# Kernel optimization log

Hardware: AMD Instinct MI355X
Metric: run time of the kernel (lower is better)

Reference implementation:

```python
import jax, jax.numpy as jnp
import numpy as np

N = 50000          # number of nodes / output rows (len(degs))
IN_C, OUT_C = 16, 16
EDGE_F = 13        # edge feature dim fed to filter net
HID = 32           # filter-net hidden width
E_NOMINAL = 800000 # target number of edges (sum of degs)


def setup_inputs() -> dict:
    rng = np.random.default_rng(0)
    # variable per-node degrees in [0, 32], adjusted so they sum exactly to E_NOMINAL
    degs = rng.integers(0, 33, size=N).astype(np.int64)
    degs[0] = max(0, degs[0] + (E_NOMINAL - int(degs.sum())))
    E = int(degs.sum())
    # segment id of each edge = destination node (equivalent to the degs-driven loop)
    idxd = np.repeat(np.arange(N, dtype=np.int32), degs)
    idxn = rng.integers(0, N, size=E).astype(np.int32)  # source node gather index

    key = jax.random.key(0)
    k1, k2, k3, k4 = jax.random.split(key, 4)
    x = jax.random.normal(k1, (N, IN_C), jnp.float32)
    edgefeats = jax.random.normal(k2, (E, EDGE_F), jnp.float32)
    # filter net: Linear(EDGE_F->HID) -> ReLU -> Linear(HID->IN_C*OUT_C)
    W1 = jax.random.normal(k3, (EDGE_F, HID), jnp.float32) / np.float32(np.sqrt(EDGE_F))
    b1 = jnp.zeros((HID,), jnp.float32)
    W2 = jax.random.normal(k4, (HID, IN_C * OUT_C), jnp.float32) / np.float32(np.sqrt(HID))
    b2 = jnp.zeros((IN_C * OUT_C,), jnp.float32)
    return {
        "x": x, "edgefeats": edgefeats,
        "W1": W1, "b1": b1, "W2": W2, "b2": b2,
        "idxn": jnp.asarray(idxn), "idxd": jnp.asarray(idxd),
        "degs": jnp.asarray(degs.astype(np.float32)),
    }


def reference(x, edgefeats, W1, b1, W2, b2, idxn, idxd, degs):
    # filter net generates a per-edge [IN_C, OUT_C] weight matrix
    h = jax.nn.relu(edgefeats @ W1 + b1)                 # [E, HID]
    w = (h @ W2 + b2).reshape(-1, IN_C, OUT_C)           # [E, IN_C, OUT_C]
    # gather source-node features and apply per-edge matvec (bmm with [E,1,IN_C])
    sel = x[idxn]                                        # [E, IN_C]
    prod = jnp.einsum('ei,eio->eo', sel, w)              # [E, OUT_C]
    # segment-mean over each node's incoming edges; degree-0 nodes -> 0
    s = jax.ops.segment_sum(prod, idxd, num_segments=N)  # [N, OUT_C]
    d = degs[:, None]
    return jnp.where(d > 0, s / jnp.maximum(d, 1.0), jnp.float32(0.0))
```

## Files before the change

### kernel.cpp

```cpp
#include <hip/hip_runtime.h>

typedef _Float16 half2v __attribute__((ext_vector_type(2)));
typedef _Float16 half8v __attribute__((ext_vector_type(8)));
typedef float   float4v __attribute__((ext_vector_type(4)));

#define INC     16
#define OUTC    16
#define EFN     13
#define HIDC    32
#define EPB     512
#define NTILES  (EPB / 16)
#define MAXSPAN 128

union H8 { half8v v; half2v h2[4]; };

#define SB(t, l, j) (((t) * 64 + (l)) * 8 + (j))

__global__ __launch_bounds__(256) void edge_kernel(
    const float* __restrict__ x,
    const float* __restrict__ edgefeats,
    const float* __restrict__ W1,
    const float* __restrict__ b1,
    const float* __restrict__ W2,
    const float* __restrict__ b2,
    const int*   __restrict__ idxn,
    const int*   __restrict__ idxd,
    const float* __restrict__ degs,
    float*       __restrict__ out,
    float*       __restrict__ wsPfirst,
    float*       __restrict__ wsPlast,
    int*         __restrict__ wsMeta,
    int E)
{
    __shared__ __align__(16) _Float16 sB[16 * 64 * 8];
    __shared__ __align__(16) _Float16 sW1h[EFN * HIDC];
    __shared__ float         lacc[MAXSPAN * OUTC];
    __shared__ int           sidxn[EPB];
    __shared__ unsigned char su[EPB];

    const int tid  = threadIdx.x;
    const int lane = tid & 63;
    const int wid  = tid >> 6;
    const int n    = lane & 15;
    const int q    = lane >> 4;

    const long b0   = (long)blockIdx.x * EPB;
    const long bEnd = (b0 + EPB < (long)E) ? (b0 + EPB) : (long)E;
    const int  d_lo = idxd[b0];
    const int  d_hi = idxd[bEnd - 1];
    const int  span = d_hi - d_lo;

    #pragma unroll
    for (int it = 0; it < 8; ++it) {
        const int idx4 = tid + it * 256;
        const float4 w4 = ((const float4*)W2)[idx4];
        const int c0 = (idx4 * 4) & 255;
        const int kk = (idx4 * 4) >> 8;
        const int t  = c0 >> 4;
        const int l0 = ((kk >> 3) << 4) + (c0 & 15);
        const int j  = kk & 7;
        sB[SB(t, l0 + 0, j)] = (_Float16)w4.x;
        sB[SB(t, l0 + 1, j)] = (_Float16)w4.y;
        sB[SB(t, l0 + 2, j)] = (_Float16)w4.z;
        sB[SB(t, l0 + 3, j)] = (_Float16)w4.w;
    }
    for (int i = tid; i < EFN * HIDC; i += 256) sW1h[i] = (_Float16)W1[i];
    #pragma unroll
    for (int it = 0; it < MAXSPAN * OUTC / 256; ++it) lacc[tid + it * 256] = 0.0f;
    {
        const int i2 = tid * 2;
        long e0 = b0 + i2, e1 = b0 + i2 + 1;
        if (e0 >= (long)E) e0 = E - 1;
        if (e1 >= (long)E) e1 = E - 1;
        sidxn[i2]     = idxn[e0];
        sidxn[i2 + 1] = idxn[e1];
        const unsigned u0 = (unsigned)(idxd[e0] - d_lo);
        const unsigned u1 = (unsigned)(idxd[e1] - d_lo);
        *(unsigned short*)&su[i2] = (unsigned short)(u0 | (u1 << 8));
    }

    half2v b1h[4];
    #pragma unroll
    for (int j2 = 0; j2 < 4; ++j2) {
        half2v t = {(_Float16)b1[q * 8 + 2 * j2], (_Float16)b1[q * 8 + 2 * j2 + 1]};
        b1h[j2] = t;
    }
    half8v bfragB2;
    #pragma unroll
    for (int j = 0; j < 8; ++j) {
        _Float16 val = (_Float16)0.f;
        if (q < 2) val = (_Float16)b2[(q * 8 + j) * 16 + n];
        bfragB2[j] = val;
    }

    __syncthreads();

    for (int t16 = wid; t16 < NTILES; t16 += 4) {
        const long base = b0 + (long)t16 * 16;
        const long eM   = base + n;
        const bool vM   = (eM < (long)E);
        const long eMc  = vM ? eM : (long)(E - 1);

        const unsigned u4  = *(const unsigned*)&su[t16 * 16 + q * 4];
        const int      node = sidxn[t16 * 16 + n];

        const float4* xp = (const float4*)(x + (size_t)node * INC);
        float4 s0 = xp[0], s1 = xp[1], s2 = xp[2], s3 = xp[3];
        if (!vM) { s0 = make_float4(0,0,0,0); s1 = s0; s2 = s0; s3 = s0; }

        half2v selh[8];
        { half2v t = {(_Float16)s0.x, (_Float16)s0.y}; selh[0] = t; }
        { half2v t = {(_Float16)s0.z, (_Float16)s0.w}; selh[1] = t; }
        { half2v t = {(_Float16)s1.x, (_Float16)s1.y}; selh[2] = t; }
        { half2v t = {(_Float16)s1.z, (_Float16)s1.w}; selh[3] = t; }
        { half2v t = {(_Float16)s2.x, (_Float16)s2.y}; selh[4] = t; }
        { half2v t = {(_Float16)s2.z, (_Float16)s2.w}; selh[5] = t; }
        { half2v t = {(_Float16)s3.x, (_Float16)s3.y}; selh[6] = t; }
        { half2v t = {(_Float16)s3.z, (_Float16)s3.w}; selh[7] = t; }

        half2v h2a[4] = {b1h[0], b1h[1], b1h[2], b1h[3]};
        const float* efp = edgefeats + (size_t)eMc * EFN;
        #pragma unroll
        for (int f = 0; f < EFN; ++f) {
            _Float16 efh = (_Float16)efp[f];
            half2v ef2 = {efh, efh};
            H8 w; w.v = *(const half8v*)&sW1h[f * HIDC + q * 8];
            h2a[0] += ef2 * w.h2[0];
            h2a[1] += ef2 * w.h2[1];
            h2a[2] += ef2 * w.h2[2];
            h2a[3] += ef2 * w.h2[3];
        }
        H8 hu;
        #pragma unroll
        for (int j2 = 0; j2 < 4; ++j2) {
            _Float16 a = h2a[j2][0], b = h2a[j2][1];
            _Float16 z = (_Float16)0.f;
            half2v t = {a > z ? a : z, b > z ? b : z};
            hu.h2[j2] = t;
        }

        float4v acc = {0.f, 0.f, 0.f, 0.f};
        #pragma unroll
        for (int t = 0; t < 16; ++t) {
            _Float16 sv = (t & 1) ? selh[t >> 1][1] : selh[t >> 1][0];
            half2v sb = {sv, sv};
            H8 a;
            a.h2[0] = sb * hu.h2[0];
            a.h2[1] = sb * hu.h2[1];
            a.h2[2] = sb * hu.h2[2];
            a.h2[3] = sb * hu.h2[3];
            const half8v bf = *(const half8v*)&sB[SB(t, lane, 0)];
            acc = __builtin_amdgcn_mfma_f32_16x16x32_f16(a.v, bf, acc, 0, 0, 0);
        }
        {
            H8 a;
            #pragma unroll
            for (int j2 = 0; j2 < 4; ++j2) {
                half2v zz = {(_Float16)0.f, (_Float16)0.f};
                a.h2[j2] = (q < 2) ? selh[q * 4 + j2] : zz;
            }
            acc = __builtin_amdgcn_mfma_f32_16x16x32_f16(a.v, bfragB2, acc, 0, 0, 0);
        }

        const unsigned rep = (u4 & 0xffu) * 0x01010101u;
        if (u4 == rep) {
            atomicAdd(&lacc[(u4 & 0xffu) * OUTC + n],
                      acc[0] + acc[1] + acc[2] + acc[3]);
        } else {
            #pragma unroll
            for (int r = 0; r < 4; ++r)
                atomicAdd(&lacc[((u4 >> (8 * r)) & 0xffu) * OUTC + n], acc[r]);
        }
    }

    __syncthreads();

    const bool first_starts = (b0 == 0)        || (idxd[b0 - 1] != d_lo);
    const bool last_ends    = (bEnd == (long)E) || (idxd[bEnd]   != d_hi);

    for (int i = tid; i < (span + 1) * OUTC; i += 256) {
        const int u = i >> 4;
        const int o = i & 15;
        const int v = d_lo + u;
        const float bin = lacc[u * OUTC + o];
        const bool starts = (u > 0)    || first_starts;
        const bool ends   = (u < span) || last_ends;
        if (starts && ends) {
            const float dg = degs[v];
            out[(size_t)v * OUTC + o] = (dg > 0.0f) ? bin / dg : 0.0f;
        } else if (!starts) {
            wsPfirst[(size_t)blockIdx.x * OUTC + o] = bin;
        } else {
            wsPlast[(size_t)blockIdx.x * OUTC + o] = bin;
        }
    }
    if (tid == 0) {
        wsMeta[blockIdx.x * 4 + 0] = d_hi;
        wsMeta[blockIdx.x * 4 + 1] = last_ends ? 1 : 0;
        wsMeta[blockIdx.x * 4 + 2] =
            (((span > 0) || first_starts) && !last_ends) ? 1 : 0;
    }
}

__global__ __launch_bounds__(256) void fixup_kernel(
    const float* __restrict__ degs,
    float*       __restrict__ out,
    const float* __restrict__ wsPfirst,
    const float* __restrict__ wsPlast,
    const int*   __restrict__ wsMeta,
    int N, int nblocks)
{
    const int t = blockIdx.x * 256 + threadIdx.x;

    if (t < nblocks && wsMeta[t * 4 + 2]) {
        const int v = wsMeta[t * 4 + 0];
        float tot[OUTC];
        #pragma unroll
        for (int o = 0; o < OUTC; ++o) tot[o] = wsPlast[(size_t)t * OUTC + o];
        for (int j = t + 1; j < nblocks; ++j) {
            #pragma unroll
            for (int o = 0; o < OUTC; ++o) tot[o] += wsPfirst[(size_t)j * OUTC + o];
            if (wsMeta[j * 4 + 0] != v || wsMeta[j * 4 + 1]) break;
        }
        const float dg = degs[v];
        #pragma unroll
        for (int o = 0; o < OUTC; ++o) out[(size_t)v * OUTC + o] = tot[o] / dg;
    }

    if (t < N && degs[t] == 0.0f) {
        float4* op = (float4*)(out + (size_t)t * OUTC);
        const float4 z = make_float4(0, 0, 0, 0);
        op[0] = z; op[1] = z; op[2] = z; op[3] = z;
    }
}

extern "C" void kernel_launch(void* const* d_in, const int* in_sizes, int n_in,
                              void* d_out, int out_size, void* d_ws, size_t ws_size,
                              hipStream_t stream)
{
    const float* x         = (const float*)d_in[0];
    const float* edgefeats = (const float*)d_in[1];
    const float* W1        = (const float*)d_in[2];
    const float* b1        = (const float*)d_in[3];
    const float* W2        = (const float*)d_in[4];
    const float* b2        = (const float*)d_in[5];
    const int*   idxn      = (const int*)d_in[6];
    const int*   idxd      = (const int*)d_in[7];
    const float* degs      = (const float*)d_in[8];

    const int E = in_sizes[6];
    const int N = in_sizes[8];
    const int nblocks = (E + EPB - 1) / EPB;

    float* wsPfirst = (float*)d_ws;
    float* wsPlast  = wsPfirst + (size_t)nblocks * OUTC;
    int*   wsMeta   = (int*)(wsPlast + (size_t)nblocks * OUTC);

    edge_kernel<<<nblocks, 256, 0, stream>>>(x, edgefeats, W1, b1, W2, b2,
                                             idxn, idxd, degs, (float*)d_out,
                                             wsPfirst, wsPlast, wsMeta, E);

    const int fthreads = (N > nblocks) ? N : nblocks;
    fixup_kernel<<<(fthreads + 255) / 256, 256, 0, stream>>>(
        degs, (float*)d_out, wsPfirst, wsPlast, wsMeta, N, nblocks);
}
```

Before: 183.9 us.

## Fuse fixup into edge kernel via last-block counter and stage edgefeats in LDS

Removes the separate fixup kernel: each block publishes its boundary partials with agent-scope atomic stores, and the last block to finish (found through an atomic counter reset by a memset) stitches together segments that cross block boundaries. Zeroing of degree-0 nodes moves into the main write loop, which now also covers gaps up to the next block's first node. Block size grows to 512 with 8 waves, edge features are staged into padded LDS as fp16 with coalesced loads, and the LDS accumulator gets a stride of 17 to avoid bank conflicts. The trade-offs are a serial tail in the last block, an extra memset launch, and higher LDS use per block.

```diff
diff --git a/kernel.cpp b/kernel.cpp
--- a/kernel.cpp
+++ b/kernel.cpp
@@ -8,15 +8,18 @@
 #define OUTC    16
 #define EFN     13
 #define HIDC    32
+#define BLOCK   512
 #define EPB     512
 #define NTILES  (EPB / 16)
 #define MAXSPAN 128
+#define LSTR    17
 
 union H8 { half8v v; half2v h2[4]; };
 
 #define SB(t, l, j) (((t) * 64 + (l)) * 8 + (j))
-
-__global__ __launch_bounds__(256) void edge_kernel(
+#define AGENT __HIP_MEMORY_SCOPE_AGENT
+
+__global__ __launch_bounds__(BLOCK, 6) void edge_kernel(
     const float* __restrict__ x,
     const float* __restrict__ edgefeats,
     const float* __restrict__ W1,
@@ -30,13 +33,16 @@
     float*       __restrict__ wsPfirst,
     float*       __restrict__ wsPlast,
     int*         __restrict__ wsMeta,
-    int E)
+    int*         __restrict__ wsCnt,
+    int E, int N, int nblocks)
 {
     __shared__ __align__(16) _Float16 sB[16 * 64 * 8];
+    __shared__ __align__(16) _Float16 sef[EPB * 16];
     __shared__ __align__(16) _Float16 sW1h[EFN * HIDC];
-    __shared__ float         lacc[MAXSPAN * OUTC];
+    __shared__ float         lacc[MAXSPAN * LSTR];
     __shared__ int           sidxn[EPB];
     __shared__ unsigned char su[EPB];
+    __shared__ int           sLastFlag;
 
     const int tid  = threadIdx.x;
     const int lane = tid & 63;
@@ -50,33 +56,31 @@
     const int  d_hi = idxd[bEnd - 1];
     const int  span = d_hi - d_lo;
 
-    #pragma unroll
-    for (int it = 0; it < 8; ++it) {
-        const int idx4 = tid + it * 256;
-        const float4 w4 = ((const float4*)W2)[idx4];
-        const int c0 = (idx4 * 4) & 255;
-        const int kk = (idx4 * 4) >> 8;
-        const int t  = c0 >> 4;
-        const int l0 = ((kk >> 3) << 4) + (c0 & 15);
-        const int j  = kk & 7;
-        sB[SB(t, l0 + 0, j)] = (_Float16)w4.x;
-        sB[SB(t, l0 + 1, j)] = (_Float16)w4.y;
-        sB[SB(t, l0 + 2, j)] = (_Float16)w4.z;
-        sB[SB(t, l0 + 3, j)] = (_Float16)w4.w;
-    }
-    for (int i = tid; i < EFN * HIDC; i += 256) sW1h[i] = (_Float16)W1[i];
-    #pragma unroll
-    for (int it = 0; it < MAXSPAN * OUTC / 256; ++it) lacc[tid + it * 256] = 0.0f;
+    for (int p = tid; p < 1024; p += BLOCK) {
+        const int t  = p >> 6, l = p & 63;
+        const int c  = t * 16 + (l & 15);
+        const int k0 = (l >> 4) * 8;
+        half8v tmp;
+        #pragma unroll
+        for (int j = 0; j < 8; ++j) tmp[j] = (_Float16)W2[(k0 + j) * 256 + c];
+        *(half8v*)&sB[p * 8] = tmp;
+    }
     {
-        const int i2 = tid * 2;
-        long e0 = b0 + i2, e1 = b0 + i2 + 1;
+        const int efTot = (int)(bEnd - b0) * EFN;
+        for (int i = tid; i < EPB * EFN; i += BLOCK) {
+            const int row = i / EFN;
+            const int col = i - row * EFN;
+            const float v = (i < efTot) ? edgefeats[b0 * EFN + i] : 0.0f;
+            sef[row * 16 + col] = (_Float16)v;
+        }
+    }
+    if (tid < EFN * HIDC) sW1h[tid] = (_Float16)W1[tid];
+    for (int i = tid; i < MAXSPAN * LSTR; i += BLOCK) lacc[i] = 0.0f;
+    {
+        long e0 = b0 + tid;
         if (e0 >= (long)E) e0 = E - 1;
-        if (e1 >= (long)E) e1 = E - 1;
-        sidxn[i2]     = idxn[e0];
-        sidxn[i2 + 1] = idxn[e1];
-        const unsigned u0 = (unsigned)(idxd[e0] - d_lo);
-        const unsigned u1 = (unsigned)(idxd[e1] - d_lo);
-        *(unsigned short*)&su[i2] = (unsigned short)(u0 | (u1 << 8));
+        sidxn[tid] = idxn[e0];
+        su[tid]    = (unsigned char)(idxd[e0] - d_lo);
     }
 
     half2v b1h[4];
@@ -95,13 +99,11 @@
 
     __syncthreads();
 
-    for (int t16 = wid; t16 < NTILES; t16 += 4) {
+    for (int t16 = wid; t16 < NTILES; t16 += 8) {
         const long base = b0 + (long)t16 * 16;
-        const long eM   = base + n;
-        const bool vM   = (eM < (long)E);
-        const long eMc  = vM ? eM : (long)(E - 1);
-
-        const unsigned u4  = *(const unsigned*)&su[t16 * 16 + q * 4];
+        const bool vM   = (base + n < (long)E);
+
+        const unsigned u4   = *(const unsigned*)&su[t16 * 16 + q * 4];
         const int      node = sidxn[t16 * 16 + n];
 
         const float4* xp = (const float4*)(x + (size_t)node * INC);
@@ -118,11 +120,14 @@
         { half2v t = {(_Float16)s3.x, (_Float16)s3.y}; selh[6] = t; }
         { half2v t = {(_Float16)s3.z, (_Float16)s3.w}; selh[7] = t; }
 
+        const int erow = (t16 * 16 + n) * 16;
+        half8v e0 = *(const half8v*)&sef[erow];
+        half8v e1 = *(const half8v*)&sef[erow + 8];
+
         half2v h2a[4] = {b1h[0], b1h[1], b1h[2], b1h[3]};
-        const float* efp = edgefeats + (size_t)eMc * EFN;
         #pragma unroll
         for (int f = 0; f < EFN; ++f) {
-            _Float16 efh = (_Float16)efp[f];
+            const _Float16 efh = (f < 8) ? e0[f] : e1[f - 8];
             half2v ef2 = {efh, efh};
             H8 w; w.v = *(const half8v*)&sW1h[f * HIDC + q * 8];
             h2a[0] += ef2 * w.h2[0];
@@ -142,7 +147,7 @@
         float4v acc = {0.f, 0.f, 0.f, 0.f};
         #pragma unroll
         for (int t = 0; t < 16; ++t) {
-            _Float16 sv = (t & 1) ? selh[t >> 1][1] : selh[t >> 1][0];
+            const _Float16 sv = (t & 1) ? selh[t >> 1][1] : selh[t >> 1][0];
             half2v sb = {sv, sv};
             H8 a;
             a.h2[0] = sb * hu.h2[0];
@@ -164,73 +169,82 @@
 
         const unsigned rep = (u4 & 0xffu) * 0x01010101u;
         if (u4 == rep) {
-            atomicAdd(&lacc[(u4 & 0xffu) * OUTC + n],
+            atomicAdd(&lacc[(u4 & 0xffu) * LSTR + n],
                       acc[0] + acc[1] + acc[2] + acc[3]);
         } else {
             #pragma unroll
             for (int r = 0; r < 4; ++r)
-                atomicAdd(&lacc[((u4 >> (8 * r)) & 0xffu) * OUTC + n], acc[r]);
-        }
-    }
-
-    __syncthreads();
-
-    const bool first_starts = (b0 == 0)        || (idxd[b0 - 1] != d_lo);
+                atomicAdd(&lacc[((u4 >> (8 * r)) & 0xffu) * LSTR + n], acc[r]);
+        }
+    }
+
+    __syncthreads();
+
+    const bool first_starts = (b0 == 0)         || (idxd[b0 - 1] != d_lo);
     const bool last_ends    = (bEnd == (long)E) || (idxd[bEnd]   != d_hi);
-
-    for (int i = tid; i < (span + 1) * OUTC; i += 256) {
+    const int  d_next = (bEnd < (long)E) ? idxd[bEnd] : N;
+    const int  span2  = d_next - d_lo;
+    const int  ucnt   = (span + 1 > span2) ? (span + 1) : span2;
+
+    for (int i = tid; i < ucnt * OUTC; i += BLOCK) {
         const int u = i >> 4;
         const int o = i & 15;
         const int v = d_lo + u;
-        const float bin = lacc[u * OUTC + o];
+        const float bin = (u <= span) ? lacc[u * LSTR + o] : 0.0f;
         const bool starts = (u > 0)    || first_starts;
         const bool ends   = (u < span) || last_ends;
         if (starts && ends) {
             const float dg = degs[v];
             out[(size_t)v * OUTC + o] = (dg > 0.0f) ? bin / dg : 0.0f;
         } else if (!starts) {
-            wsPfirst[(size_t)blockIdx.x * OUTC + o] = bin;
+            __hip_atomic_store(&wsPfirst[(size_t)blockIdx.x * OUTC + o], bin,
+                               __ATOMIC_RELAXED, AGENT);
         } else {
-            wsPlast[(size_t)blockIdx.x * OUTC + o] = bin;
-        }
-    }
+            __hip_atomic_store(&wsPlast[(size_t)blockIdx.x * OUTC + o], bin,
+                               __ATOMIC_RELAXED, AGENT);
+        }
+    }
+    if (blockIdx.x == 0)
+        for (int i = tid; i < d_lo * OUTC; i += BLOCK) out[i] = 0.0f;
+
     if (tid == 0) {
-        wsMeta[blockIdx.x * 4 + 0] = d_hi;
-        wsMeta[blockIdx.x * 4 + 1] = last_ends ? 1 : 0;
-        wsMeta[blockIdx.x * 4 + 2] =
-            (((span > 0) || first_starts) && !last_ends) ? 1 : 0;
-    }
-}
-
-__global__ __launch_bounds__(256) void fixup_kernel(
-    const float* __restrict__ degs,
-    float*       __restrict__ out,
-    const float* __restrict__ wsPfirst,
-    const float* __restrict__ wsPlast,
-    const int*   __restrict__ wsMeta,
-    int N, int nblocks)
-{
-    const int t = blockIdx.x * 256 + threadIdx.x;
-
-    if (t < nblocks && wsMeta[t * 4 + 2]) {
-        const int v = wsMeta[t * 4 + 0];
-        float tot[OUTC];
-        #pragma unroll
-        for (int o = 0; o < OUTC; ++o) tot[o] = wsPlast[(size_t)t * OUTC + o];
-        for (int j = t + 1; j < nblocks; ++j) {
-            #pragma unroll
-            for (int o = 0; o < OUTC; ++o) tot[o] += wsPfirst[(size_t)j * OUTC + o];
-            if (wsMeta[j * 4 + 0] != v || wsMeta[j * 4 + 1]) break;
-        }
-        const float dg = degs[v];
-        #pragma unroll
-        for (int o = 0; o < OUTC; ++o) out[(size_t)v * OUTC + o] = tot[o] / dg;
-    }
-
-    if (t < N && degs[t] == 0.0f) {
-        float4* op = (float4*)(out + (size_t)t * OUTC);
-        const float4 z = make_float4(0, 0, 0, 0);
-        op[0] = z; op[1] = z; op[2] = z; op[3] = z;
+        __hip_atomic_store(&wsMeta[blockIdx.x * 4 + 0], d_hi, __ATOMIC_RELAXED, AGENT);
+        __hip_atomic_store(&wsMeta[blockIdx.x * 4 + 1], last_ends ? 1 : 0, __ATOMIC_RELAXED, AGENT);
+        const int owner = (((span > 0) || first_starts) && !last_ends) ? 1 : 0;
+        __hip_atomic_store(&wsMeta[blockIdx.x * 4 + 2], owner, __ATOMIC_RELAXED, AGENT);
+    }
+
+    __syncthreads();
+    if (tid == 0) {
+        const int old = __hip_atomic_fetch_add(wsCnt, 1, __ATOMIC_ACQ_REL, AGENT);
+        sLastFlag = (old == nblocks - 1) ? 1 : 0;
+    }
+    __syncthreads();
+
+    if (sLastFlag) {
+        for (int t = tid; t < nblocks; t += BLOCK) {
+            if (!__hip_atomic_load(&wsMeta[t * 4 + 2], __ATOMIC_RELAXED, AGENT))
+                continue;
+            const int v = __hip_atomic_load(&wsMeta[t * 4 + 0], __ATOMIC_RELAXED, AGENT);
+            float tot[OUTC];
+            #pragma unroll
+            for (int o = 0; o < OUTC; ++o)
+                tot[o] = __hip_atomic_load(&wsPlast[(size_t)t * OUTC + o],
+                                           __ATOMIC_RELAXED, AGENT);
+            for (int j = t + 1; j < nblocks; ++j) {
+                #pragma unroll
+                for (int o = 0; o < OUTC; ++o)
+                    tot[o] += __hip_atomic_load(&wsPfirst[(size_t)j * OUTC + o],
+                                                __ATOMIC_RELAXED, AGENT);
+                if (__hip_atomic_load(&wsMeta[j * 4 + 0], __ATOMIC_RELAXED, AGENT) != v ||
+                    __hip_atomic_load(&wsMeta[j * 4 + 1], __ATOMIC_RELAXED, AGENT))
+                    break;
+            }
+            const float dg = degs[v];
+            #pragma unroll
+            for (int o = 0; o < OUTC; ++o)
+                out[(size_t)v * OUTC + o] = tot[o] / dg;
+        }
     }
 }
 
@@ -252,15 +266,15 @@
     const int N = in_sizes[8];
     const int nblocks = (E + EPB - 1) / EPB;
 
-    float* wsPfirst = (float*)d_ws;
+    int*   wsCnt    = (int*)d_ws;
+    float* wsPfirst = (float*)((char*)d_ws + 16);
     float* wsPlast  = wsPfirst + (size_t)nblocks * OUTC;
     int*   wsMeta   = (int*)(wsPlast + (size_t)nblocks * OUTC);
 
-    edge_kernel<<<nblocks, 256, 0, stream>>>(x, edgefeats, W1, b1, W2, b2,
-                                             idxn, idxd, degs, (float*)d_out,
-                                             wsPfirst, wsPlast, wsMeta, E);
-
-    const int fthreads = (N > nblocks) ? N : nblocks;
-    fixup_kernel<<<(fthreads + 255) / 256, 256, 0, stream>>>(
-        degs, (float*)d_out, wsPfirst, wsPlast, wsMeta, N, nblocks);
+    hipMemsetAsync(wsCnt, 0, sizeof(int), stream);
+
+    edge_kernel<<<nblocks, BLOCK, 0, stream>>>(x, edgefeats, W1, b1, W2, b2,
+                                               idxn, idxd, degs, (float*)d_out,
+                                               wsPfirst, wsPlast, wsMeta, wsCnt,
+                                               E, N, nblocks);
 }
```

Result: slower. 456.0 us (+147.9%).
